# Kernel optimization log

Measured on AMD Instinct MI355X. Metric: run time of the kernel, lower is better.

Reference implementation:

```python
import jax, jax.numpy as jnp
import numpy as np

B = 4096
NC = 64        # n_concepts
NT = 16        # n_tasks
H = 256        # prior_units (prior_layers = 1)
HID = 256      # prior_hids = [256, 256]
K = 20         # n_components
IN = 3 * NC + NT + 1        # GRU input size = 209
MLP_IN = H + 3 * NC + NT    # rnn_out input = 464
LOG_2PI = float(np.log(2.0 * np.pi))


def setup_inputs() -> dict:
    key = jax.random.key(0)
    ks = jax.random.split(key, 16)
    s = 0.05
    inp = {
        "z": jax.random.normal(ks[0], (B, NC), jnp.float32),
        "c": jax.random.normal(ks[1], (B, NC + NT), jnp.float32),
        "b": (jax.random.uniform(ks[2], (B, NC)) < 0.5).astype(jnp.float32),
        "m": (jax.random.uniform(ks[3], (B, NC)) < 0.5).astype(jnp.float32),
        # GRU (PyTorch layout: gates ordered r, z, n)
        "W_ih": jax.random.normal(ks[4], (3 * H, IN), jnp.float32) * s,
        "W_hh": jax.random.normal(ks[5], (3 * H, H), jnp.float32) * s,
        "b_ih": jax.random.normal(ks[6], (3 * H,), jnp.float32) * s,
        "b_hh": jax.random.normal(ks[7], (3 * H,), jnp.float32) * s,
        # rnn_out MLP: Linear(464,256)+Tanh, Linear(256,256)+Tanh, Linear(256,3K)
        "W1": jax.random.normal(ks[8], (HID, MLP_IN), jnp.float32) * s,
        "b1": jax.random.normal(ks[9], (HID,), jnp.float32) * s,
        "W2": jax.random.normal(ks[10], (HID, HID), jnp.float32) * s,
        "b2": jax.random.normal(ks[11], (HID,), jnp.float32) * s,
        "W3": jax.random.normal(ks[12], (3 * K, HID), jnp.float32) * s,
        "b3": jax.random.normal(ks[13], (3 * K,), jnp.float32) * s,
    }
    return inp


def _logp(z, c, b, m, W_ih, W_hh, b_ih, b_hh, W1, b1, W2, b2, W3, b3):
    Bsz, d = z.shape
    cbm = jnp.concatenate([c, b, m], axis=1)               # [B, 3*NC+NT]
    # z input at step t is -1 for t=0, else z[:, t-1]
    z_prev = jnp.concatenate(
        [-jnp.ones((Bsz, 1), z.dtype), z[:, :-1]], axis=1)  # [B, d]
    # Precompute the input-gate projections for all steps without
    # materializing the full [d, B, IN] sequence tensor:
    # column 0 of W_ih multiplies z_prev; the rest multiplies cbm.
    gi_cbm = cbm @ W_ih[:, 1:].T + b_ih                    # [B, 3H]
    gi = gi_cbm[None, :, :] + z_prev.T[:, :, None] * W_ih[:, 0][None, None, :]  # [d, B, 3H]

    def gru_step(h, gi_t):
        gh = h @ W_hh.T + b_hh
        gi_r, gi_u, gi_n = jnp.split(gi_t, 3, axis=-1)
        gh_r, gh_u, gh_n = jnp.split(gh, 3, axis=-1)
        r = jax.nn.sigmoid(gi_r + gh_r)
        u = jax.nn.sigmoid(gi_u + gh_u)
        n = jnp.tanh(gi_n + r * gh_n)
        h_new = (1.0 - u) * n + u * h
        return h_new, h_new

    h0 = jnp.zeros((Bsz, W_hh.shape[1]), z.dtype)
    _, hs = jax.lax.scan(gru_step, h0, gi)                 # [d, B, H]
    hs = jnp.transpose(hs, (1, 0, 2))                      # [B, d, H]

    feat = jnp.concatenate(
        [hs, jnp.broadcast_to(cbm[:, None, :], (Bsz, d, cbm.shape[1]))],
        axis=2)                                            # [B, d, MLP_IN]
    h1 = jnp.tanh(feat @ W1.T + b1)
    h2 = jnp.tanh(h1 @ W2.T + b2)
    params = h2 @ W3.T + b3                                # [B, d, 3K]

    logits, means, lsigmas = jnp.split(params, 3, axis=-1)
    t = z[..., None]                                       # [B, d, 1]
    log_norm = -lsigmas - 0.5 * LOG_2PI
    diff = (t - means) * jnp.exp(-lsigmas)
    log_kernel = -0.5 * jnp.square(diff)
    log_like = (jax.nn.logsumexp(log_kernel + log_norm + logits, axis=-1)
                - jax.nn.logsumexp(logits, axis=-1))       # [B, d]

    query = m * (1.0 - b)
    mask = jnp.sort(query, axis=1)[:, ::-1]                # descending sort of values
    return jnp.sum(log_like * mask, axis=1)                # [B]


def reference(z, c, b, m, W_ih, W_hh, b_ih, b_hh, W1, b1, W2, b2, W3, b3):
    return _logp(z, c, b, m, W_ih, W_hh, b_ih, b_hh,
                 W1, b1, W2, b2, W3, b3)
```

## Files before the change

### kernel.cpp

```cpp
#include <hip/hip_runtime.h>
#include <hip/hip_bf16.h>

#define BATCH  4096
#define NCC    64
#define HDIM   256
#define G3     768
#define NROW   (BATCH*NCC)
#define NK     20
#define LOG2PI 1.8378770664093453f

typedef __attribute__((ext_vector_type(8))) short bf16x8;
typedef __attribute__((ext_vector_type(4))) float f32x4;

__device__ __forceinline__ float sigm(float x) { return 1.0f/(1.0f + __expf(-x)); }
__device__ __forceinline__ float tanh_fast(float x) { return 1.0f - 2.0f/(__expf(2.0f*x) + 1.0f); }
__device__ __forceinline__ unsigned short f2bf(float x) {
  __hip_bfloat16 h = __float2bfloat16(x);
  return __builtin_bit_cast(unsigned short, h);
}
__device__ __forceinline__ int swz(int r) { return (r & 7) ^ ((r & 8) >> 2); }

typedef const __attribute__((address_space(1))) unsigned int glb_u32;
typedef __attribute__((address_space(3))) unsigned int lds_u32;
__device__ __forceinline__ void gload16(const unsigned short* g, unsigned short* l) {
  __builtin_amdgcn_global_load_lds((glb_u32*)g, (lds_u32*)l, 16, 0, 0);
}

#define MFMA_BA(d, a, b) \
  asm("v_mfma_f32_16x16x32_bf16 %0, %1, %2, %0" : "+v"(d) : "v"(a), "a"(b))
#define MFMA_BV(d, a, b) \
  asm("v_mfma_f32_16x16x32_bf16 %0, %1, %2, %0" : "+v"(d) : "v"(a), "v"(b))

__global__ __launch_bounds__(256) void k_cvtall(
    const float* __restrict__ c, const float* __restrict__ bv,
    const float* __restrict__ mv, const float* __restrict__ W_ih,
    const float* __restrict__ W_hh, const float* __restrict__ W1,
    const float* __restrict__ W2, const float* __restrict__ W3,
    unsigned short* __restrict__ cbmB, unsigned short* __restrict__ CW,
    unsigned short* __restrict__ WhhB, unsigned short* __restrict__ W1aB,
    unsigned short* __restrict__ W2B, unsigned short* __restrict__ W3pB,
    float* __restrict__ w0) {
  int idx = blockIdx.x*256 + threadIdx.x;
  if (idx < 1048576) {
    int row = idx >> 8, k = idx & 255;
    float v = 0.f;
    if (k < 80)       v = c [row*80 + k];
    else if (k < 144) v = bv[row*64 + (k-80)];
    else if (k < 208) v = mv[row*64 + (k-144)];
    cbmB[idx] = f2bf(v);
    return;
  }
  idx -= 1048576;
  if (idx < 262144) {
    int n = idx >> 8, k = idx & 255;
    float v = 0.f;
    if (n < 768) { if (k < 208) v = W_ih[n*209 + 1 + k]; }
    else         { if (k < 208) v = W1[(n-768)*464 + 256 + k]; }
    CW[idx] = f2bf(v);
    return;
  }
  idx -= 262144;
  if (idx < 196608) { WhhB[idx] = f2bf(W_hh[idx]); return; }
  idx -= 196608;
  if (idx < 65536) { int n = idx>>8, k = idx&255; W1aB[idx] = f2bf(W1[n*464+k]); return; }
  idx -= 65536;
  if (idx < 65536) { W2B[idx] = f2bf(W2[idx]); return; }
  idx -= 65536;
  if (idx < 16384) {
    int n = idx >> 8;
    float v = 0.f;
    if (n < 60) v = W3[idx];
    W3pB[idx] = f2bf(v);
    return;
  }
  idx -= 16384;
  if (idx < 768) w0[idx] = W_ih[idx*209];
}

__global__ __launch_bounds__(512) void k_pre(
    const unsigned short* __restrict__ A, const unsigned short* __restrict__ Bw,
    const float* __restrict__ b_ih, const float* __restrict__ b_hh,
    const float* __restrict__ b1,
    float* __restrict__ gi, float* __restrict__ P1) {
  __shared__ __align__(16) unsigned short As[128*64];
  __shared__ __align__(16) unsigned short Bs[128*64];
  int tid = threadIdx.x;
  int rb = blockIdx.x >> 3, cb = blockIdx.x & 7;
  long row0 = (long)rb * 128;
  int n0 = cb * 128;
  int wv = tid >> 6, lane = tid & 63;
  int lq = lane >> 4, l16 = lane & 15;
  int wrg = wv & 3, wcg = wv >> 2;
  const int w64 = tid & ~63;
  f32x4 acc[2][4];
#pragma unroll
  for (int i = 0; i < 2; ++i)
#pragma unroll
    for (int j = 0; j < 4; ++j) acc[i][j] = (f32x4){0.f,0.f,0.f,0.f};
  for (int kb = 0; kb < 256; kb += 64) {
#pragma unroll
    for (int i = 0; i < 2; ++i) {
      int s = i*512 + tid;
      int r = s >> 3, cg = (s & 7) ^ (r & 7);
      gload16(&A[(row0 + r)*256 + kb + cg*8],        &As[(i*512 + w64)*8]);
      gload16(&Bw[(long)(n0 + r)*256 + kb + cg*8],   &Bs[(i*512 + w64)*8]);
    }
    __syncthreads();
#pragma unroll
    for (int kc = 0; kc < 2; ++kc) {
      int csel = kc*4 + lq;
      bf16x8 af[2];
#pragma unroll
      for (int rt = 0; rt < 2; ++rt) {
        int r = wrg*32 + rt*16 + l16;
        af[rt] = *(const bf16x8*)&As[r*64 + ((csel ^ (r & 7)))*8];
      }
#pragma unroll
      for (int ct = 0; ct < 4; ++ct) {
        int n = wcg*64 + ct*16 + l16;
        bf16x8 bfr = *(const bf16x8*)&Bs[n*64 + ((csel ^ (n & 7)))*8];
        acc[0][ct] = __builtin_amdgcn_mfma_f32_16x16x32_bf16(af[0], bfr, acc[0][ct], 0, 0, 0);
        acc[1][ct] = __builtin_amdgcn_mfma_f32_16x16x32_bf16(af[1], bfr, acc[1][ct], 0, 0, 0);
      }
    }
    __syncthreads();
  }
#pragma unroll
  for (int rt = 0; rt < 2; ++rt)
#pragma unroll
    for (int q = 0; q < 4; ++q) {
      long row = row0 + wrg*32 + rt*16 + lq*4 + q;
#pragma unroll
      for (int ct = 0; ct < 4; ++ct) {
        int n = n0 + wcg*64 + ct*16 + l16;
        float v = acc[rt][ct][q];
        if (n < 512)      gi[row*G3 + n] = v + b_ih[n] + b_hh[n];
        else if (n < 768) gi[row*G3 + n] = v + b_ih[n];
        else              P1[row*256 + (n-768)] = v + b1[n-768];
      }
    }
}

__global__ __attribute__((amdgpu_flat_work_group_size(256, 256)))
__attribute__((amdgpu_waves_per_eu(1, 1)))
void k_gru(
    const float* __restrict__ z, const float* __restrict__ gi,
    const unsigned short* __restrict__ WhhB, const float* __restrict__ b_hh,
    const float* __restrict__ w0, unsigned short* __restrict__ hs) {
  __shared__ __align__(16) unsigned short hbf[2*16*256];
  __shared__ __align__(16) float gis[768*20];
  __shared__ __align__(16) float zs[64*16];
  __shared__ float wls[768 + 256];
  int tid = threadIdx.x;
  int wv = tid >> 6, lane = tid & 63;
  int lq = lane >> 4, l16 = lane & 15;
  int row0 = blockIdx.x * 16;

  bf16x8 wfA[2][4][8];
  bf16x8 wfN[4][8];
#pragma unroll
  for (int g = 0; g < 2; ++g)
#pragma unroll
    for (int cf = 0; cf < 4; ++cf)
#pragma unroll
      for (int ks = 0; ks < 8; ++ks) {
        wfA[g][cf][ks] = *(const bf16x8*)&WhhB[
            (long)(g*256 + wv*64 + cf*16 + l16)*256 + ks*32 + lq*8];
        asm volatile("" : "+a"(wfA[g][cf][ks]));
      }
#pragma unroll
  for (int cf = 0; cf < 4; ++cf)
#pragma unroll
    for (int ks = 0; ks < 8; ++ks) {
      wfN[cf][ks] = *(const bf16x8*)&WhhB[
          (long)(512 + wv*64 + cf*16 + l16)*256 + ks*32 + lq*8];
      asm volatile("" : "+v"(wfN[cf][ks]));
    }

  for (int i = tid; i < 768; i += 256) wls[i] = w0[i];
  for (int i = tid; i < 256; i += 256) wls[768 + i] = b_hh[512 + i];
  for (int i = tid; i < 1024; i += 256) {
    int t = i >> 4, r = i & 15;
    zs[i] = z[(row0+r)*64 + t];
  }
#pragma unroll
  for (int i = 0; i < 12; ++i) {
    int s = i*256 + tid;
    int r = s / 192, c4 = (s - r*192)*4;
    float4 v = *(const float4*)&gi[(long)(row0+r)*768 + c4];
    gis[(c4+0)*20 + r] = v.x;
    gis[(c4+1)*20 + r] = v.y;
    gis[(c4+2)*20 + r] = v.z;
    gis[(c4+3)*20 + r] = v.w;
  }
  for (int i = tid; i < 2048; i += 256) ((unsigned int*)hbf)[i] = 0u;

  float hp[4][4];
#pragma unroll
  for (int i = 0; i < 4; ++i)
#pragma unroll
    for (int j = 0; j < 4; ++j) hp[i][j] = 0.f;

  const int s7 = l16 & 7;
  const int arow = l16*256;
  const int r4 = lq*4;
  const int cr = tid >> 4;
  const int chA = tid & 15;
  const int chB = chA + 16;
  const int cswz = cr & 7;
  unsigned short* cbase = hs + (long)(row0+cr)*64*256 + chA*8;
  __syncthreads();

#pragma unroll 1
  for (int t = 0; t < 64; ++t) {
    const int co = (t & 1) << 12;
    const int no = co ^ 4096;
    float zp[4];
    {
      float4 zv4 = *(const float4*)&zs[(t ? (t-1) : 0)*16 + r4];
#pragma unroll
      for (int q = 0; q < 4; ++q) zp[q] = t ? (&zv4.x)[q] : -1.0f;
    }
    if (t) {
      uint4 c0 = *(const uint4*)&hbf[co + cr*256 + ((chA ^ cswz))*8];
      uint4 c1 = *(const uint4*)&hbf[co + cr*256 + ((chB ^ cswz))*8];
      *(uint4*)(cbase + (t-1)*256)       = c0;
      *(uint4*)(cbase + (t-1)*256 + 128) = c1;
    }
#pragma unroll
    for (int hf = 0; hf < 2; ++hf) {
      f32x4 acc[3][2];
#pragma unroll
      for (int c2 = 0; c2 < 2; ++c2) {
        int cf = hf*2 + c2;
        int hc = wv*64 + cf*16 + l16;
        f32x4 gR = *(const f32x4*)&gis[hc*20 + r4];
        f32x4 gU = *(const f32x4*)&gis[(256+hc)*20 + r4];
        float w0r = wls[hc], w0u = wls[256+hc], bn = wls[768+hc];
#pragma unroll
        for (int q = 0; q < 4; ++q) {
          acc[0][c2][q] = gR[q] + zp[q]*w0r;
          acc[1][c2][q] = gU[q] + zp[q]*w0u;
          acc[2][c2][q] = bn;
        }
      }
      asm volatile("s_nop 1"
        : "+v"(acc[0][0]), "+v"(acc[0][1]), "+v"(acc[1][0]),
          "+v"(acc[1][1]), "+v"(acc[2][0]), "+v"(acc[2][1]));
#pragma unroll
      for (int ks = 0; ks < 8; ++ks) {
        bf16x8 af = *(const bf16x8*)&hbf[co + arow + ((ks*4+lq) ^ s7)*8];
#pragma unroll
        for (int c2 = 0; c2 < 2; ++c2) {
          int cf = hf*2 + c2;
          MFMA_BA(acc[0][c2], af, wfA[0][cf][ks]);
          MFMA_BA(acc[1][c2], af, wfA[1][cf][ks]);
          MFMA_BV(acc[2][c2], af, wfN[cf][ks]);
        }
      }
      asm volatile("s_nop 7\n\ts_nop 7"
        : "+v"(acc[0][0]), "+v"(acc[0][1]), "+v"(acc[1][0]),
          "+v"(acc[1][1]), "+v"(acc[2][0]), "+v"(acc[2][1]));
#pragma unroll
      for (int c2 = 0; c2 < 2; ++c2) {
        int cf = hf*2 + c2;
        int hc = wv*64 + cf*16 + l16;
        int hchunk = hc >> 3, hlow = hc & 7;
        float w0n = wls[512 + hc];
        f32x4 gN = *(const f32x4*)&gis[(512+hc)*20 + r4];
#pragma unroll
        for (int q = 0; q < 4; ++q) {
          int r = r4 + q;
          float rr = sigm(acc[0][c2][q]);
          float uu = sigm(acc[1][c2][q]);
          float nn = tanh_fast(gN[q] + zp[q]*w0n + rr*acc[2][c2][q]);
          float hn = uu*(hp[cf][q] - nn) + nn;
          hp[cf][q] = hn;
          hbf[no + r*256 + ((hchunk ^ (r & 7)))*8 + hlow] = f2bf(hn);
        }
      }
    }
    __syncthreads();
  }
  {
    uint4 c0 = *(const uint4*)&hbf[0 + cr*256 + ((chA ^ cswz))*8];
    uint4 c1 = *(const uint4*)&hbf[0 + cr*256 + ((chB ^ cswz))*8];
    *(uint4*)(cbase + 63*256)       = c0;
    *(uint4*)(cbase + 63*256 + 128) = c1;
  }
}

__global__ __launch_bounds__(512) void k_mlp(
    const unsigned short* __restrict__ A, const unsigned short* __restrict__ W1aB,
    const float* __restrict__ P1, const unsigned short* __restrict__ W2B,
    const float* __restrict__ b2, const unsigned short* __restrict__ W3pB,
    const float* __restrict__ b3, const float* __restrict__ z,
    float* __restrict__ ll) {
  __shared__ __align__(16) unsigned short As[128*64];
  __shared__ __align__(16) unsigned short Bs[256*64];
  __shared__ __align__(16) unsigned short H[128*256];
  int tid = threadIdx.x;
  long row0 = (long)blockIdx.x * 128;
  int wv = tid >> 6, lane = tid & 63;
  int lq = lane >> 4, l16 = lane & 15;
  int wrg = wv & 3, wcg = wv >> 2;
  const int w64 = tid & ~63;
  f32x4 acc[2][8];

#pragma unroll
  for (int i = 0; i < 2; ++i)
#pragma unroll
    for (int j = 0; j < 8; ++j) acc[i][j] = (f32x4){0.f,0.f,0.f,0.f};
  for (int kb = 0; kb < 256; kb += 64) {
#pragma unroll
    for (int i = 0; i < 2; ++i) {
      int s = i*512 + tid;
      int r = s >> 3, cg = (s & 7) ^ (r & 7);
      gload16(&A[(row0 + r)*256 + kb + cg*8], &As[(i*512 + w64)*8]);
    }
#pragma unroll
    for (int i = 0; i < 4; ++i) {
      int s = i*512 + tid;
      int r = s >> 3, cg = (s & 7) ^ (r & 7);
      gload16(&W1aB[(long)r*256 + kb + cg*8], &Bs[(i*512 + w64)*8]);
    }
    __syncthreads();
#pragma unroll
    for (int kc = 0; kc < 2; ++kc) {
      int csel = kc*4 + lq;
      bf16x8 af[2];
#pragma unroll
      for (int rt = 0; rt < 2; ++rt) {
        int r = wrg*32 + rt*16 + l16;
        af[rt] = *(const bf16x8*)&As[r*64 + ((csel ^ (r & 7)))*8];
      }
#pragma unroll
      for (int ct = 0; ct < 8; ++ct) {
        int n = wcg*128 + ct*16 + l16;
        bf16x8 bfr = *(const bf16x8*)&Bs[n*64 + ((csel ^ (n & 7)))*8];
        acc[0][ct] = __builtin_amdgcn_mfma_f32_16x16x32_bf16(af[0], bfr, acc[0][ct], 0, 0, 0);
        acc[1][ct] = __builtin_amdgcn_mfma_f32_16x16x32_bf16(af[1], bfr, acc[1][ct], 0, 0, 0);
      }
    }
    __syncthreads();
  }
#pragma unroll
  for (int rt = 0; rt < 2; ++rt)
#pragma unroll
    for (int q = 0; q < 4; ++q) {
      int lr = wrg*32 + rt*16 + lq*4 + q;
      long row = row0 + lr;
#pragma unroll
      for (int ct = 0; ct < 8; ++ct) {
        int n = wcg*128 + ct*16 + l16;
        float b = P1[(row >> 6)*256 + n];
        H[lr*256 + (((n >> 3) ^ swz(lr))*8 + (n & 7))] =
            f2bf(tanh_fast(acc[rt][ct][q] + b));
      }
    }
  __syncthreads();

#pragma unroll
  for (int i = 0; i < 2; ++i)
#pragma unroll
    for (int j = 0; j < 8; ++j) acc[i][j] = (f32x4){0.f,0.f,0.f,0.f};
  for (int kb = 0; kb < 256; kb += 64) {
#pragma unroll
    for (int i = 0; i < 4; ++i) {
      int s = i*512 + tid;
      int r = s >> 3, cg = (s & 7) ^ (r & 7);
      gload16(&W2B[(long)r*256 + kb + cg*8], &Bs[(i*512 + w64)*8]);
    }
    __syncthreads();
#pragma unroll
    for (int kc = 0; kc < 2; ++kc) {
      int csel = kc*4 + lq;
      int chunk = (kb >> 3) + csel;
      bf16x8 af[2];
#pragma unroll
      for (int rt = 0; rt < 2; ++rt) {
        int r = wrg*32 + rt*16 + l16;
        af[rt] = *(const bf16x8*)&H[r*256 + ((chunk ^ swz(r)))*8];
      }
#pragma unroll
      for (int ct = 0; ct < 8; ++ct) {
        int n = wcg*128 + ct*16 + l16;
        bf16x8 bfr = *(const bf16x8*)&Bs[n*64 + ((csel ^ (n & 7)))*8];
        acc[0][ct] = __builtin_amdgcn_mfma_f32_16x16x32_bf16(af[0], bfr, acc[0][ct], 0, 0, 0);
        acc[1][ct] = __builtin_amdgcn_mfma_f32_16x16x32_bf16(af[1], bfr, acc[1][ct], 0, 0, 0);
      }
    }
    __syncthreads();
  }
#pragma unroll
  for (int rt = 0; rt < 2; ++rt)
#pragma unroll
    for (int q = 0; q < 4; ++q) {
      int lr = wrg*32 + rt*16 + lq*4 + q;
#pragma unroll
      for (int ct = 0; ct < 8; ++ct) {
        int n = wcg*128 + ct*16 + l16;
        H[lr*256 + (((n >> 3) ^ swz(lr))*8 + (n & 7))] =
            f2bf(tanh_fast(acc[rt][ct][q] + b2[n]));
      }
    }
  __syncthreads();
#pragma unroll
  for (int i = 0; i < 4; ++i) {
    int s = i*512 + tid;
    int r = s >> 5, cc = s & 31;
    *(uint4*)&Bs[r*256 + ((cc ^ swz(r)))*8] = *(const uint4*)&W3pB[r*256 + cc*8];
  }
  __syncthreads();

  f32x4 pacc[4];
#pragma unroll
  for (int j = 0; j < 4; ++j) pacc[j] = (f32x4){0.f,0.f,0.f,0.f};
#pragma unroll
  for (int ks = 0; ks < 8; ++ks) {
    int chunk = ks*4 + lq;
    int ar = wv*16 + l16;
    bf16x8 af = *(const bf16x8*)&H[ar*256 + ((chunk ^ swz(ar)))*8];
#pragma unroll
    for (int ct = 0; ct < 4; ++ct) {
      int br = ct*16 + l16;
      bf16x8 bfr = *(const bf16x8*)&Bs[br*256 + ((chunk ^ swz(br)))*8];
      pacc[ct] = __builtin_amdgcn_mfma_f32_16x16x32_bf16(af, bfr, pacc[ct], 0, 0, 0);
    }
  }
  float* Ps = (float*)&H[wv*16*256];
#pragma unroll
  for (int ct = 0; ct < 4; ++ct) {
    int n = ct*16 + l16;
    float b = (n < 60) ? b3[n] : 0.0f;
#pragma unroll
    for (int q = 0; q < 4; ++q)
      Ps[(lq*4 + q)*68 + n] = pacc[ct][q] + b;
  }
  if (lane < 16) {
    long grow = row0 + wv*16 + lane;
    float zv = z[grow];
    const float* p = &Ps[lane*68];
    float mx1 = -1e30f;
#pragma unroll
    for (int i = 0; i < NK; ++i) mx1 = fmaxf(mx1, p[i]);
    float s1 = 0.0f;
#pragma unroll
    for (int i = 0; i < NK; ++i) s1 += __expf(p[i] - mx1);
    float lse1 = mx1 + __logf(s1);
    float a[NK];
    float mx2 = -1e30f;
#pragma unroll
    for (int i = 0; i < NK; ++i) {
      float lg = p[i], me = p[20+i], ls = p[40+i];
      float e = __expf(-ls);
      float d = (zv - me) * e;
      float ai = -0.5f*d*d - ls - 0.5f*LOG2PI + lg;
      a[i] = ai;
      mx2 = fmaxf(mx2, ai);
    }
    float s2 = 0.0f;
#pragma unroll
    for (int i = 0; i < NK; ++i) s2 += __expf(a[i] - mx2);
    float lse2 = mx2 + __logf(s2);
    ll[grow] = lse2 - lse1;
  }
}

__global__ __launch_bounds__(256) void k_final(const float* __restrict__ bv,
    const float* __restrict__ mv, const float* __restrict__ ll,
    float* __restrict__ out) {
  int tid = threadIdx.x;
  int wave = tid >> 6, lane = tid & 63;
  int b = blockIdx.x*4 + wave;
  float q = mv[b*64 + lane] * (1.0f - bv[b*64 + lane]);
  unsigned long long bal = __ballot(q > 0.5f);
  int S = __popcll(bal);
  float val = (lane < S) ? ll[(long)b*64 + lane] : 0.0f;
#pragma unroll
  for (int off = 32; off > 0; off >>= 1) val += __shfl_down(val, off);
  if (lane == 0) out[b] = val;
}

extern "C" void kernel_launch(void* const* d_in, const int* in_sizes, int n_in,
                              void* d_out, int out_size, void* d_ws, size_t ws_size,
                              hipStream_t stream) {
  const float* z    = (const float*)d_in[0];
  const float* c    = (const float*)d_in[1];
  const float* bv   = (const float*)d_in[2];
  const float* mv   = (const float*)d_in[3];
  const float* W_ih = (const float*)d_in[4];
  const float* W_hh = (const float*)d_in[5];
  const float* b_ih = (const float*)d_in[6];
  const float* b_hh = (const float*)d_in[7];
  const float* W1   = (const float*)d_in[8];
  const float* b1   = (const float*)d_in[9];
  const float* W2   = (const float*)d_in[10];
  const float* b2   = (const float*)d_in[11];
  const float* W3   = (const float*)d_in[12];
  const float* b3   = (const float*)d_in[13];
  float* out = (float*)d_out;

  char* p = (char*)d_ws;
  auto alloc = [&](size_t bytes) {
    char* q = p;
    p += (bytes + 255) & ~(size_t)255;
    return q;
  };
  unsigned short* cbmB = (unsigned short*)alloc((size_t)BATCH*256*2);
  unsigned short* CW   = (unsigned short*)alloc((size_t)1024*256*2);
  unsigned short* WhhB = (unsigned short*)alloc((size_t)G3*256*2);
  unsigned short* W1aB = (unsigned short*)alloc((size_t)256*256*2);
  unsigned short* W2B  = (unsigned short*)alloc((size_t)256*256*2);
  unsigned short* W3pB = (unsigned short*)alloc((size_t)64*256*2);
  float* w0 = (float*)alloc((size_t)G3*4);
  float* gi = (float*)alloc((size_t)BATCH*G3*4);
  float* P1 = (float*)alloc((size_t)BATCH*256*4);
  float* ll = (float*)alloc((size_t)NROW*4);
  unsigned short* hs = (unsigned short*)alloc((size_t)NROW*HDIM*2);

  k_cvtall<<<6468, 256, 0, stream>>>(c, bv, mv, W_ih, W_hh, W1, W2, W3,
                                     cbmB, CW, WhhB, W1aB, W2B, W3pB, w0);
  k_pre<<<256, 512, 0, stream>>>(cbmB, CW, b_ih, b_hh, b1, gi, P1);
  k_gru<<<256, 256, 0, stream>>>(z, gi, WhhB, b_hh, w0, hs);
  k_mlp<<<NROW/128, 512, 0, stream>>>(hs, W1aB, P1, W2B, b2, W3pB, b3, z, ll);
  k_final<<<BATCH/4, 256, 0, stream>>>(bv, mv, ll, out);
}
```

Before: 497.9 us.

## Split GRU hidden columns across eight waves instead of four per block

```diff
diff --git a/kernel.cpp b/kernel.cpp
--- a/kernel.cpp
+++ b/kernel.cpp
@@ -141,8 +141,8 @@
     }
 }
 
-__global__ __attribute__((amdgpu_flat_work_group_size(256, 256)))
-__attribute__((amdgpu_waves_per_eu(1, 1)))
+__global__ __attribute__((amdgpu_flat_work_group_size(512, 512)))
+__attribute__((amdgpu_waves_per_eu(2, 2)))
 void k_gru(
     const float* __restrict__ z, const float* __restrict__ gi,
     const unsigned short* __restrict__ WhhB, const float* __restrict__ b_hh,
@@ -156,36 +156,27 @@
   int lq = lane >> 4, l16 = lane & 15;
   int row0 = blockIdx.x * 16;
 
-  bf16x8 wfA[2][4][8];
-  bf16x8 wfN[4][8];
-#pragma unroll
-  for (int g = 0; g < 2; ++g)
-#pragma unroll
-    for (int cf = 0; cf < 4; ++cf)
+  bf16x8 wf[3][2][8];
+#pragma unroll
+  for (int g = 0; g < 3; ++g)
+#pragma unroll
+    for (int cf = 0; cf < 2; ++cf)
 #pragma unroll
       for (int ks = 0; ks < 8; ++ks) {
-        wfA[g][cf][ks] = *(const bf16x8*)&WhhB[
-            (long)(g*256 + wv*64 + cf*16 + l16)*256 + ks*32 + lq*8];
-        asm volatile("" : "+a"(wfA[g][cf][ks]));
-      }
-#pragma unroll
-  for (int cf = 0; cf < 4; ++cf)
-#pragma unroll
-    for (int ks = 0; ks < 8; ++ks) {
-      wfN[cf][ks] = *(const bf16x8*)&WhhB[
-          (long)(512 + wv*64 + cf*16 + l16)*256 + ks*32 + lq*8];
-      asm volatile("" : "+v"(wfN[cf][ks]));
-    }
-
-  for (int i = tid; i < 768; i += 256) wls[i] = w0[i];
-  for (int i = tid; i < 256; i += 256) wls[768 + i] = b_hh[512 + i];
-  for (int i = tid; i < 1024; i += 256) {
+        wf[g][cf][ks] = *(const bf16x8*)&WhhB[
+            (long)(g*256 + wv*32 + cf*16 + l16)*256 + ks*32 + lq*8];
+        asm volatile("" : "+a"(wf[g][cf][ks]));
+      }
+
+  for (int i = tid; i < 768; i += 512) wls[i] = w0[i];
+  for (int i = tid; i < 256; i += 512) wls[768 + i] = b_hh[512 + i];
+  for (int i = tid; i < 1024; i += 512) {
     int t = i >> 4, r = i & 15;
     zs[i] = z[(row0+r)*64 + t];
   }
 #pragma unroll
-  for (int i = 0; i < 12; ++i) {
-    int s = i*256 + tid;
+  for (int i = 0; i < 6; ++i) {
+    int s = i*512 + tid;
     int r = s / 192, c4 = (s - r*192)*4;
     float4 v = *(const float4*)&gi[(long)(row0+r)*768 + c4];
     gis[(c4+0)*20 + r] = v.x;
@@ -193,22 +184,21 @@
     gis[(c4+2)*20 + r] = v.z;
     gis[(c4+3)*20 + r] = v.w;
   }
-  for (int i = tid; i < 2048; i += 256) ((unsigned int*)hbf)[i] = 0u;
-
-  float hp[4][4];
-#pragma unroll
-  for (int i = 0; i < 4; ++i)
+  for (int i = tid; i < 2048; i += 512) ((unsigned int*)hbf)[i] = 0u;
+
+  float hp[2][4];
+#pragma unroll
+  for (int i = 0; i < 2; ++i)
 #pragma unroll
     for (int j = 0; j < 4; ++j) hp[i][j] = 0.f;
 
   const int s7 = l16 & 7;
   const int arow = l16*256;
   const int r4 = lq*4;
-  const int cr = tid >> 4;
-  const int chA = tid & 15;
-  const int chB = chA + 16;
+  const int cr = tid >> 5;
+  const int ch = tid & 31;
   const int cswz = cr & 7;
-  unsigned short* cbase = hs + (long)(row0+cr)*64*256 + chA*8;
+  unsigned short* cbase = hs + (long)(row0+cr)*64*256 + ch*8;
   __syncthreads();
 
 #pragma unroll 1
@@ -222,71 +212,61 @@
       for (int q = 0; q < 4; ++q) zp[q] = t ? (&zv4.x)[q] : -1.0f;
     }
     if (t) {
-      uint4 c0 = *(const uint4*)&hbf[co + cr*256 + ((chA ^ cswz))*8];
-      uint4 c1 = *(const uint4*)&hbf[co + cr*256 + ((chB ^ cswz))*8];
-      *(uint4*)(cbase + (t-1)*256)       = c0;
-      *(uint4*)(cbase + (t-1)*256 + 128) = c1;
-    }
-#pragma unroll
-    for (int hf = 0; hf < 2; ++hf) {
-      f32x4 acc[3][2];
-#pragma unroll
-      for (int c2 = 0; c2 < 2; ++c2) {
-        int cf = hf*2 + c2;
-        int hc = wv*64 + cf*16 + l16;
-        f32x4 gR = *(const f32x4*)&gis[hc*20 + r4];
-        f32x4 gU = *(const f32x4*)&gis[(256+hc)*20 + r4];
-        float w0r = wls[hc], w0u = wls[256+hc], bn = wls[768+hc];
-#pragma unroll
-        for (int q = 0; q < 4; ++q) {
-          acc[0][c2][q] = gR[q] + zp[q]*w0r;
-          acc[1][c2][q] = gU[q] + zp[q]*w0u;
-          acc[2][c2][q] = bn;
-        }
-      }
-      asm volatile("s_nop 1"
-        : "+v"(acc[0][0]), "+v"(acc[0][1]), "+v"(acc[1][0]),
-          "+v"(acc[1][1]), "+v"(acc[2][0]), "+v"(acc[2][1]));
-#pragma unroll
-      for (int ks = 0; ks < 8; ++ks) {
-        bf16x8 af = *(const bf16x8*)&hbf[co + arow + ((ks*4+lq) ^ s7)*8];
-#pragma unroll
-        for (int c2 = 0; c2 < 2; ++c2) {
-          int cf = hf*2 + c2;
-          MFMA_BA(acc[0][c2], af, wfA[0][cf][ks]);
-          MFMA_BA(acc[1][c2], af, wfA[1][cf][ks]);
-          MFMA_BV(acc[2][c2], af, wfN[cf][ks]);
-        }
-      }
-      asm volatile("s_nop 7\n\ts_nop 7"
-        : "+v"(acc[0][0]), "+v"(acc[0][1]), "+v"(acc[1][0]),
-          "+v"(acc[1][1]), "+v"(acc[2][0]), "+v"(acc[2][1]));
-#pragma unroll
-      for (int c2 = 0; c2 < 2; ++c2) {
-        int cf = hf*2 + c2;
-        int hc = wv*64 + cf*16 + l16;
-        int hchunk = hc >> 3, hlow = hc & 7;
-        float w0n = wls[512 + hc];
-        f32x4 gN = *(const f32x4*)&gis[(512+hc)*20 + r4];
-#pragma unroll
-        for (int q = 0; q < 4; ++q) {
-          int r = r4 + q;
-          float rr = sigm(acc[0][c2][q]);
-          float uu = sigm(acc[1][c2][q]);
-          float nn = tanh_fast(gN[q] + zp[q]*w0n + rr*acc[2][c2][q]);
-          float hn = uu*(hp[cf][q] - nn) + nn;
-          hp[cf][q] = hn;
-          hbf[no + r*256 + ((hchunk ^ (r & 7)))*8 + hlow] = f2bf(hn);
-        }
+      uint4 c0 = *(const uint4*)&hbf[co + cr*256 + ((ch ^ cswz))*8];
+      *(uint4*)(cbase + (t-1)*256) = c0;
+    }
+    f32x4 acc[3][2];
+#pragma unroll
+    for (int cf = 0; cf < 2; ++cf) {
+      int hc = wv*32 + cf*16 + l16;
+      f32x4 gR = *(const f32x4*)&gis[hc*20 + r4];
+      f32x4 gU = *(const f32x4*)&gis[(256+hc)*20 + r4];
+      float w0r = wls[hc], w0u = wls[256+hc], bn = wls[768+hc];
+#pragma unroll
+      for (int q = 0; q < 4; ++q) {
+        acc[0][cf][q] = gR[q] + zp[q]*w0r;
+        acc[1][cf][q] = gU[q] + zp[q]*w0u;
+        acc[2][cf][q] = bn;
+      }
+    }
+    asm volatile("s_nop 1"
+      : "+v"(acc[0][0]), "+v"(acc[0][1]), "+v"(acc[1][0]),
+        "+v"(acc[1][1]), "+v"(acc[2][0]), "+v"(acc[2][1]));
+#pragma unroll
+    for (int ks = 0; ks < 8; ++ks) {
+      bf16x8 af = *(const bf16x8*)&hbf[co + arow + ((ks*4+lq) ^ s7)*8];
+#pragma unroll
+      for (int cf = 0; cf < 2; ++cf) {
+        MFMA_BA(acc[0][cf], af, wf[0][cf][ks]);
+        MFMA_BA(acc[1][cf], af, wf[1][cf][ks]);
+        MFMA_BA(acc[2][cf], af, wf[2][cf][ks]);
+      }
+    }
+    asm volatile("s_nop 7\n\ts_nop 7"
+      : "+v"(acc[0][0]), "+v"(acc[0][1]), "+v"(acc[1][0]),
+        "+v"(acc[1][1]), "+v"(acc[2][0]), "+v"(acc[2][1]));
+#pragma unroll
+    for (int cf = 0; cf < 2; ++cf) {
+      int hc = wv*32 + cf*16 + l16;
+      int hchunk = hc >> 3, hlow = hc & 7;
+      float w0n = wls[512 + hc];
+      f32x4 gN = *(const f32x4*)&gis[(512+hc)*20 + r4];
+#pragma unroll
+      for (int q = 0; q < 4; ++q) {
+        int r = r4 + q;
+        float rr = sigm(acc[0][cf][q]);
+        float uu = sigm(acc[1][cf][q]);
+        float nn = tanh_fast(gN[q] + zp[q]*w0n + rr*acc[2][cf][q]);
+        float hn = uu*(hp[cf][q] - nn) + nn;
+        hp[cf][q] = hn;
+        hbf[no + r*256 + ((hchunk ^ (r & 7)))*8 + hlow] = f2bf(hn);
       }
     }
     __syncthreads();
   }
   {
-    uint4 c0 = *(const uint4*)&hbf[0 + cr*256 + ((chA ^ cswz))*8];
-    uint4 c1 = *(const uint4*)&hbf[0 + cr*256 + ((chB ^ cswz))*8];
-    *(uint4*)(cbase + 63*256)       = c0;
-    *(uint4*)(cbase + 63*256 + 128) = c1;
+    uint4 c0 = *(const uint4*)&hbf[0 + cr*256 + ((ch ^ cswz))*8];
+    *(uint4*)(cbase + 63*256) = c0;
   }
 }
 
@@ -522,7 +502,7 @@
   k_cvtall<<<6468, 256, 0, stream>>>(c, bv, mv, W_ih, W_hh, W1, W2, W3,
                                      cbmB, CW, WhhB, W1aB, W2B, W3pB, w0);
   k_pre<<<256, 512, 0, stream>>>(cbmB, CW, b_ih, b_hh, b1, gi, P1);
-  k_gru<<<256, 256, 0, stream>>>(z, gi, WhhB, b_hh, w0, hs);
+  k_gru<<<256, 512, 0, stream>>>(z, gi, WhhB, b_hh, w0, hs);
   k_mlp<<<NROW/128, 512, 0, stream>>>(hs, W1aB, P1, W2B, b2, W3pB, b3, z, ll);
   k_final<<<BATCH/4, 256, 0, stream>>>(bv, mv, ll, out);
 }
```

New measurement: 525.0 us. +5.4%, slower.

## Interleave two 16-row batch groups per GRU block to overlap MFMA and gates

Applied to the files above, without the earlier changes.

```diff
diff --git a/kernel.cpp b/kernel.cpp
--- a/kernel.cpp
+++ b/kernel.cpp
@@ -147,14 +147,14 @@
     const float* __restrict__ z, const float* __restrict__ gi,
     const unsigned short* __restrict__ WhhB, const float* __restrict__ b_hh,
     const float* __restrict__ w0, unsigned short* __restrict__ hs) {
-  __shared__ __align__(16) unsigned short hbf[2*16*256];
-  __shared__ __align__(16) float gis[768*20];
-  __shared__ __align__(16) float zs[64*16];
+  __shared__ __align__(16) unsigned short hbf[4*4096];
+  __shared__ __align__(16) float gis[768*36];
+  __shared__ __align__(16) float zs[64*32];
   __shared__ float wls[768 + 256];
   int tid = threadIdx.x;
   int wv = tid >> 6, lane = tid & 63;
   int lq = lane >> 4, l16 = lane & 15;
-  int row0 = blockIdx.x * 16;
+  int row0 = blockIdx.x * 32;
 
   bf16x8 wfA[2][4][8];
   bf16x8 wfN[4][8];
@@ -179,27 +179,22 @@
 
   for (int i = tid; i < 768; i += 256) wls[i] = w0[i];
   for (int i = tid; i < 256; i += 256) wls[768 + i] = b_hh[512 + i];
-  for (int i = tid; i < 1024; i += 256) {
-    int t = i >> 4, r = i & 15;
+  for (int i = tid; i < 2048; i += 256) {
+    int t = i >> 5, r = i & 31;
     zs[i] = z[(row0+r)*64 + t];
   }
 #pragma unroll
-  for (int i = 0; i < 12; ++i) {
+  for (int i = 0; i < 24; ++i) {
     int s = i*256 + tid;
     int r = s / 192, c4 = (s - r*192)*4;
     float4 v = *(const float4*)&gi[(long)(row0+r)*768 + c4];
-    gis[(c4+0)*20 + r] = v.x;
-    gis[(c4+1)*20 + r] = v.y;
-    gis[(c4+2)*20 + r] = v.z;
-    gis[(c4+3)*20 + r] = v.w;
-  }
-  for (int i = tid; i < 2048; i += 256) ((unsigned int*)hbf)[i] = 0u;
-
-  float hp[4][4];
-#pragma unroll
-  for (int i = 0; i < 4; ++i)
-#pragma unroll
-    for (int j = 0; j < 4; ++j) hp[i][j] = 0.f;
+    int gb = (r & 16) + (r & 15);
+    gis[(c4+0)*36 + gb] = v.x;
+    gis[(c4+1)*36 + gb] = v.y;
+    gis[(c4+2)*36 + gb] = v.z;
+    gis[(c4+3)*36 + gb] = v.w;
+  }
+  for (int i = tid; i < 8192; i += 256) ((unsigned int*)hbf)[i] = 0u;
 
   const int s7 = l16 & 7;
   const int arow = l16*256;
@@ -208,86 +203,118 @@
   const int chA = tid & 15;
   const int chB = chA + 16;
   const int cswz = cr & 7;
-  unsigned short* cbase = hs + (long)(row0+cr)*64*256 + chA*8;
-  __syncthreads();
-
-#pragma unroll 1
-  for (int t = 0; t < 64; ++t) {
-    const int co = (t & 1) << 12;
-    const int no = co ^ 4096;
-    float zp[4];
-    {
-      float4 zv4 = *(const float4*)&zs[(t ? (t-1) : 0)*16 + r4];
-#pragma unroll
-      for (int q = 0; q < 4; ++q) zp[q] = t ? (&zv4.x)[q] : -1.0f;
-    }
-    if (t) {
-      uint4 c0 = *(const uint4*)&hbf[co + cr*256 + ((chA ^ cswz))*8];
-      uint4 c1 = *(const uint4*)&hbf[co + cr*256 + ((chB ^ cswz))*8];
-      *(uint4*)(cbase + (t-1)*256)       = c0;
-      *(uint4*)(cbase + (t-1)*256 + 128) = c1;
-    }
-#pragma unroll
-    for (int hf = 0; hf < 2; ++hf) {
-      f32x4 acc[3][2];
+  unsigned short* cbA = hs + (long)(row0+cr)*64*256 + chA*8;
+  unsigned short* cbB = hs + (long)(row0+16+cr)*64*256 + chA*8;
+
+  auto initacc = [&](f32x4 (&acc)[3][2], int grp, int hf, int t) {
+    f32x4 zpv;
+    if (t) zpv = *(const f32x4*)&zs[(t-1)*32 + grp*16 + r4];
+    else   zpv = (f32x4){-1.f,-1.f,-1.f,-1.f};
+#pragma unroll
+    for (int c2 = 0; c2 < 2; ++c2) {
+      int cf = hf*2 + c2;
+      int hc = wv*64 + cf*16 + l16;
+      f32x4 gR = *(const f32x4*)&gis[hc*36 + grp*16 + r4];
+      f32x4 gU = *(const f32x4*)&gis[(256+hc)*36 + grp*16 + r4];
+      float w0r = wls[hc], w0u = wls[256+hc], bn = wls[768+hc];
+#pragma unroll
+      for (int q = 0; q < 4; ++q) {
+        acc[0][c2][q] = gR[q] + zpv[q]*w0r;
+        acc[1][c2][q] = gU[q] + zpv[q]*w0u;
+        acc[2][c2][q] = bn;
+      }
+    }
+  };
+  auto mfma8 = [&](f32x4 (&acc)[3][2], int grp, int hf, int rdbuf) {
+    asm volatile("s_nop 1"
+      : "+v"(acc[0][0]), "+v"(acc[0][1]), "+v"(acc[1][0]),
+        "+v"(acc[1][1]), "+v"(acc[2][0]), "+v"(acc[2][1]));
+    int base = grp*8192 + rdbuf*4096;
+#pragma unroll
+    for (int ks = 0; ks < 8; ++ks) {
+      bf16x8 af = *(const bf16x8*)&hbf[base + arow + ((ks*4+lq) ^ s7)*8];
 #pragma unroll
       for (int c2 = 0; c2 < 2; ++c2) {
         int cf = hf*2 + c2;
-        int hc = wv*64 + cf*16 + l16;
-        f32x4 gR = *(const f32x4*)&gis[hc*20 + r4];
-        f32x4 gU = *(const f32x4*)&gis[(256+hc)*20 + r4];
-        float w0r = wls[hc], w0u = wls[256+hc], bn = wls[768+hc];
-#pragma unroll
-        for (int q = 0; q < 4; ++q) {
-          acc[0][c2][q] = gR[q] + zp[q]*w0r;
-          acc[1][c2][q] = gU[q] + zp[q]*w0u;
-          acc[2][c2][q] = bn;
-        }
-      }
-      asm volatile("s_nop 1"
-        : "+v"(acc[0][0]), "+v"(acc[0][1]), "+v"(acc[1][0]),
-          "+v"(acc[1][1]), "+v"(acc[2][0]), "+v"(acc[2][1]));
-#pragma unroll
-      for (int ks = 0; ks < 8; ++ks) {
-        bf16x8 af = *(const bf16x8*)&hbf[co + arow + ((ks*4+lq) ^ s7)*8];
-#pragma unroll
-        for (int c2 = 0; c2 < 2; ++c2) {
-          int cf = hf*2 + c2;
-          MFMA_BA(acc[0][c2], af, wfA[0][cf][ks]);
-          MFMA_BA(acc[1][c2], af, wfA[1][cf][ks]);
-          MFMA_BV(acc[2][c2], af, wfN[cf][ks]);
-        }
-      }
-      asm volatile("s_nop 7\n\ts_nop 7"
-        : "+v"(acc[0][0]), "+v"(acc[0][1]), "+v"(acc[1][0]),
-          "+v"(acc[1][1]), "+v"(acc[2][0]), "+v"(acc[2][1]));
-#pragma unroll
-      for (int c2 = 0; c2 < 2; ++c2) {
-        int cf = hf*2 + c2;
-        int hc = wv*64 + cf*16 + l16;
-        int hchunk = hc >> 3, hlow = hc & 7;
-        float w0n = wls[512 + hc];
-        f32x4 gN = *(const f32x4*)&gis[(512+hc)*20 + r4];
-#pragma unroll
-        for (int q = 0; q < 4; ++q) {
-          int r = r4 + q;
-          float rr = sigm(acc[0][c2][q]);
-          float uu = sigm(acc[1][c2][q]);
-          float nn = tanh_fast(gN[q] + zp[q]*w0n + rr*acc[2][c2][q]);
-          float hn = uu*(hp[cf][q] - nn) + nn;
-          hp[cf][q] = hn;
-          hbf[no + r*256 + ((hchunk ^ (r & 7)))*8 + hlow] = f2bf(hn);
-        }
-      }
-    }
-    __syncthreads();
-  }
+        MFMA_BA(acc[0][c2], af, wfA[0][cf][ks]);
+        MFMA_BA(acc[1][c2], af, wfA[1][cf][ks]);
+        MFMA_BV(acc[2][c2], af, wfN[cf][ks]);
+      }
+    }
+  };
+  auto gates = [&](f32x4 (&acc)[3][2], int grp, int hf, int s) {
+    int wrb = grp*8192 + (s&1)*4096;
+    int hpb = grp*8192 + ((s-1)&1)*4096;
+    f32x4 zpv;
+    if (s) zpv = *(const f32x4*)&zs[(s-1)*32 + grp*16 + r4];
+    else   zpv = (f32x4){-1.f,-1.f,-1.f,-1.f};
+#pragma unroll
+    for (int c2 = 0; c2 < 2; ++c2) {
+      int cf = hf*2 + c2;
+      int hc = wv*64 + cf*16 + l16;
+      int hchunk = hc >> 3, hlow = hc & 7;
+      float w0n = wls[512 + hc];
+      f32x4 gN = *(const f32x4*)&gis[(512+hc)*36 + grp*16 + r4];
+#pragma unroll
+      for (int q = 0; q < 4; ++q) {
+        int r = r4 + q;
+        int off = r*256 + ((hchunk ^ (r & 7)))*8 + hlow;
+        unsigned int hpbits = (unsigned int)hbf[hpb + off] << 16;
+        float hp = __builtin_bit_cast(float, hpbits);
+        float rr = sigm(acc[0][c2][q]);
+        float uu = sigm(acc[1][c2][q]);
+        float nn = tanh_fast(gN[q] + zpv[q]*w0n + rr*acc[2][c2][q]);
+        float hn = uu*(hp - nn) + nn;
+        hbf[wrb + off] = f2bf(hn);
+      }
+    }
+  };
+  auto copyg = [&](int grp, int t) {
+    int base = grp*8192 + ((t-1)&1)*4096;
+    unsigned short* cb = grp ? cbB : cbA;
+    uint4 c0 = *(const uint4*)&hbf[base + cr*256 + ((chA ^ cswz))*8];
+    uint4 c1 = *(const uint4*)&hbf[base + cr*256 + ((chB ^ cswz))*8];
+    *(uint4*)(cb + (t-1)*256)       = c0;
+    *(uint4*)(cb + (t-1)*256 + 128) = c1;
+  };
+
+  f32x4 accA0[3][2], accA1[3][2], accB0[3][2], accB1[3][2];
+  __syncthreads();
+
   {
-    uint4 c0 = *(const uint4*)&hbf[0 + cr*256 + ((chA ^ cswz))*8];
-    uint4 c1 = *(const uint4*)&hbf[0 + cr*256 + ((chB ^ cswz))*8];
-    *(uint4*)(cbase + 63*256)       = c0;
-    *(uint4*)(cbase + 63*256 + 128) = c1;
-  }
+    f32x4 tmp[3][2];
+    initacc(tmp, 0, 0, 0); gates(tmp, 0, 0, 0);
+    initacc(tmp, 0, 1, 0); gates(tmp, 0, 1, 0);
+    initacc(accB0, 1, 0, 0);
+    initacc(accB1, 1, 1, 0);
+  }
+  __syncthreads();
+
+#pragma unroll 1
+  for (int t = 1; t < 64; ++t) {
+    const int rd = (t-1) & 1;
+    initacc(accA0, 0, 0, t); mfma8(accA0, 0, 0, rd);
+    copyg(0, t);
+    gates(accB0, 1, 0, t-1);
+    initacc(accA1, 0, 1, t); mfma8(accA1, 0, 1, rd);
+    gates(accB1, 1, 1, t-1);
+    __syncthreads();
+    initacc(accB0, 1, 0, t); mfma8(accB0, 1, 0, rd);
+    copyg(1, t);
+    gates(accA0, 0, 0, t);
+    initacc(accB1, 1, 1, t); mfma8(accB1, 1, 1, rd);
+    gates(accA1, 0, 1, t);
+    __syncthreads();
+  }
+
+  asm volatile("s_nop 7\n\ts_nop 7"
+    : "+v"(accB0[0][0]), "+v"(accB0[1][0]), "+v"(accB0[2][0]),
+      "+v"(accB1[0][0]), "+v"(accB1[1][0]), "+v"(accB1[2][0]));
+  gates(accB0, 1, 0, 63);
+  gates(accB1, 1, 1, 63);
+  copyg(0, 64);
+  __syncthreads();
+  copyg(1, 64);
 }
 
 __global__ __launch_bounds__(512) void k_mlp(
@@ -522,7 +549,7 @@
   k_cvtall<<<6468, 256, 0, stream>>>(c, bv, mv, W_ih, W_hh, W1, W2, W3,
                                      cbmB, CW, WhhB, W1aB, W2B, W3pB, w0);
   k_pre<<<256, 512, 0, stream>>>(cbmB, CW, b_ih, b_hh, b1, gi, P1);
-  k_gru<<<256, 256, 0, stream>>>(z, gi, WhhB, b_hh, w0, hs);
+  k_gru<<<128, 256, 0, stream>>>(z, gi, WhhB, b_hh, w0, hs);
   k_mlp<<<NROW/128, 512, 0, stream>>>(hs, W1aB, P1, W2B, b2, W3pB, b3, z, ll);
   k_final<<<BATCH/4, 256, 0, stream>>>(bv, mv, ll, out);
 }
```

Result: slower. 1.155 ms (+132.0%).
